# Performance work log

Hardware: AMD Instinct MI355X
Metric: run time of the kernel (lower is better)

Reference implementation:

```python
import jax, jax.numpy as jnp
import numpy as np

N = 100000
E = 1600000
D_IN = 128
D_H = 128


def _glorot(key, shape):
    fan_in, fan_out = shape[1], shape[0]
    lim = np.sqrt(6.0 / (fan_in + fan_out))
    return jax.random.uniform(key, shape, jnp.float32, -lim, lim)


def setup_inputs() -> dict:
    key = jax.random.key(0)
    ks = jax.random.split(key, 12)
    x = jax.random.normal(ks[0], (N, D_IN), jnp.float32)
    edge_index = jax.random.randint(ks[1], (2, E), 0, N, jnp.int64)
    return {
        "x": x,
        "edge_index": edge_index,
        # lin1, lin2 (nn.Linear: y = x @ W.T + b)
        "W1": _glorot(ks[2], (D_H, D_IN)),
        "b1": jnp.zeros((D_H,), jnp.float32),
        "W2": _glorot(ks[3], (D_H, D_H)),
        "b2": jnp.zeros((D_H,), jnp.float32),
        # SAGEConv1: lin_l (neighbors, with bias), lin_r (root, no bias)
        "c1_Wl": _glorot(ks[4], (D_H, D_H)),
        "c1_bl": jnp.zeros((D_H,), jnp.float32),
        "c1_Wr": _glorot(ks[5], (D_H, D_H)),
        # SAGEConv2
        "c2_Wl": _glorot(ks[6], (D_H, D_H)),
        "c2_bl": jnp.zeros((D_H,), jnp.float32),
        "c2_Wr": _glorot(ks[7], (D_H, D_H)),
    }


def _sage_conv(h, src, dst, Wl, bl, Wr, num_nodes):
    # PyG SAGEConv (mean aggr): out = lin_l(mean_{j in N(i)} h_j) + lin_r(h_i)
    msgs = h[src]  # [E, D] gather
    agg = jax.ops.segment_sum(msgs, dst, num_segments=num_nodes)  # [N, D]
    deg = jax.ops.segment_sum(jnp.ones((src.shape[0],), h.dtype), dst,
                              num_segments=num_nodes)
    mean = agg / jnp.maximum(deg, 1.0)[:, None]
    return mean @ Wl.T + bl + h @ Wr.T


def reference(x, edge_index, W1, b1, W2, b2,
              c1_Wl, c1_bl, c1_Wr, c2_Wl, c2_bl, c2_Wr):
    src, dst = edge_index[0], edge_index[1]
    n = x.shape[0]
    h = jax.nn.relu(x @ W1.T + b1)
    h = jax.nn.relu(_sage_conv(h, src, dst, c1_Wl, c1_bl, c1_Wr, n))
    h = jax.nn.relu(h @ W2.T + b2)
    h = jax.nn.relu(_sage_conv(h, src, dst, c2_Wl, c2_bl, c2_Wr, n))
    return h
```

## Files before the change

kernel.cpp:

```cpp
#include <hip/hip_runtime.h>
#include <hip/hip_bf16.h>

#define NN 100000
#define EE 1600000
#define DD 128

#define BSH 9
#define NBUK ((NN + 511) / 512)
#define EPB 8192
#define PGRID ((EE + EPB - 1) / EPB)

typedef __attribute__((ext_vector_type(8))) _Float16 half8;
typedef __attribute__((ext_vector_type(4))) _Float16 half4;
typedef __attribute__((ext_vector_type(2))) _Float16 half2v;
typedef __attribute__((ext_vector_type(4))) float f32x4;

__device__ inline int detect64(const long long* __restrict__ ei64) {
    long long v = ei64[threadIdx.x & 63];
    return __all(v >= 0 && v < (long long)NN);
}

__device__ inline int load_edge(const int* ei32, const long long* ei64, int is64, size_t pos) {
    return is64 ? (int)ei64[pos] : ei32[pos];
}

__global__ __launch_bounds__(1024) void k_bhist(const int* __restrict__ ei32,
                                                const long long* __restrict__ ei64,
                                                int* __restrict__ bh) {
    __shared__ int h[NBUK];
    int t = threadIdx.x;
    int is64 = detect64(ei64);
    if (t < NBUK) h[t] = 0;
    __syncthreads();
    int base = blockIdx.x * EPB;
    int end = min(base + EPB, EE);
    for (int e = base + t; e < end; e += 1024) {
        int d = load_edge(ei32, ei64, is64, (size_t)EE + e);
        atomicAdd(&h[d >> BSH], 1);
    }
    __syncthreads();
    if (t < NBUK) bh[blockIdx.x * 256 + t] = h[t];
}

__global__ __launch_bounds__(256) void k_bscan(const int* __restrict__ bh,
                                               int* __restrict__ bbase,
                                               int* __restrict__ bcur) {
    __shared__ int sm[256];
    int t = threadIdx.x;
    int v = 0;
    if (t < NBUK)
        for (int b = 0; b < PGRID; ++b) v += bh[b * 256 + t];
    sm[t] = v;
    __syncthreads();
    for (int off = 1; off < 256; off <<= 1) {
        int u = (t >= off) ? sm[t - off] : 0;
        __syncthreads();
        sm[t] += u;
        __syncthreads();
    }
    if (t < NBUK) {
        int b = sm[t] - v;
        bbase[t] = b;
        bcur[t] = b;
    }
    if (t == 0) bbase[NBUK] = EE;
}

__global__ __launch_bounds__(1024) void k_part(const int* __restrict__ ei32,
                                               const long long* __restrict__ ei64,
                                               int* __restrict__ bcur,
                                               unsigned* __restrict__ eb) {
    __shared__ int h[NBUK];
    __shared__ int cbase[NBUK];
    int t = threadIdx.x;
    int is64 = detect64(ei64);
    if (t < NBUK) h[t] = 0;
    __syncthreads();
    int base = blockIdx.x * EPB;
    int end = min(base + EPB, EE);
    for (int e = base + t; e < end; e += 1024) {
        int d = load_edge(ei32, ei64, is64, (size_t)EE + e);
        atomicAdd(&h[d >> BSH], 1);
    }
    __syncthreads();
    if (t < NBUK && h[t] > 0) cbase[t] = atomicAdd(&bcur[t], h[t]);
    __syncthreads();
    if (t < NBUK) h[t] = 0;
    __syncthreads();
    for (int e = base + t; e < end; e += 1024) {
        int s = load_edge(ei32, ei64, is64, (size_t)e);
        int d = load_edge(ei32, ei64, is64, (size_t)EE + e);
        int b = d >> BSH;
        int slot = atomicAdd(&h[b], 1);
        eb[cbase[b] + slot] = (unsigned)s | ((unsigned)(d & 511) << 17);
    }
}

__global__ __launch_bounds__(1024) void k_bucket(const unsigned* __restrict__ eb,
                                                 const int* __restrict__ bbase,
                                                 int* __restrict__ rp,
                                                 int* __restrict__ ssrc) {
    __shared__ int ncnt[512];
    __shared__ int cur[512];
    int b = blockIdx.x, t = threadIdx.x;
    int ebeg = bbase[b], eend = bbase[b + 1];
    int nodeBase = b << BSH;
    int nNodes = min(512, NN - nodeBase);
    if (t < 512) ncnt[t] = 0;
    __syncthreads();
    for (int i = ebeg + t; i < eend; i += 1024) {
        unsigned v = eb[i];
        atomicAdd(&ncnt[v >> 17], 1);
    }
    __syncthreads();
    int own = (t < 512) ? ncnt[t] : 0;
    for (int off = 1; off < 512; off <<= 1) {
        int u = (t >= off && t < 512) ? ncnt[t - off] : 0;
        __syncthreads();
        if (t < 512) ncnt[t] += u;
        __syncthreads();
    }
    if (t < 512) {
        int excl = ncnt[t] - own;
        cur[t] = ebeg + excl;
        if (t < nNodes) rp[nodeBase + t] = ebeg + excl;
    }
    __syncthreads();
    for (int i = ebeg + t; i < eend; i += 1024) {
        unsigned v = eb[i];
        int slot = atomicAdd(&cur[v >> 17], 1);
        ssrc[slot] = (int)(v & 0x1FFFFu);
    }
    if (b == 0 && t == 0) rp[NN] = EE;
}

#define WSTR 136

__device__ inline void stageW(const float* __restrict__ Wg, _Float16* sW, int t) {
#pragma unroll
    for (int i = 0; i < 16; ++i) {
        int c = t + i * 256;
        int n = c >> 5, j = c & 31;
        float4 w = ((const float4*)Wg)[c];
        half4 o;
        o[0] = (_Float16)w.x; o[1] = (_Float16)w.y;
        o[2] = (_Float16)w.z; o[3] = (_Float16)w.w;
        *(half4*)(sW + n * WSTR + j * 4) = o;
    }
}

template <bool DUAL, bool AF16, bool OF16>
__global__ __launch_bounds__(256) void k_gemm(const void* __restrict__ A,
                                              const float* __restrict__ W1g,
                                              const void* __restrict__ A2,
                                              const float* __restrict__ W2g,
                                              const float* __restrict__ bias,
                                              void* __restrict__ out) {
    __shared__ _Float16 sW[128 * WSTR];
    int t = threadIdx.x;
    int wave = t >> 6;
    int lane = t & 63;
    int lr = lane & 15;
    int lk = lane >> 4;
    int rowBase = blockIdx.x * 128 + wave * 32;

    f32x4 acc[2][8];
#pragma unroll
    for (int mt = 0; mt < 2; ++mt)
#pragma unroll
        for (int nt = 0; nt < 8; ++nt) acc[mt][nt] = (f32x4){0.f, 0.f, 0.f, 0.f};

    const int NPASS = DUAL ? 2 : 1;
    for (int pass = 0; pass < NPASS; ++pass) {
        const float* Wg = pass ? W2g : W1g;
        const void* Ap = pass ? A2 : A;
        if (pass) __syncthreads();
        stageW(Wg, sW, t);
        __syncthreads();

#pragma unroll
        for (int ks = 0; ks < 4; ++ks) {
            int kf = ks * 32 + lk * 8;
            half8 b[8];
#pragma unroll
            for (int nt = 0; nt < 8; ++nt)
                b[nt] = *(const half8*)(sW + (nt * 16 + lr) * WSTR + kf);
#pragma unroll
            for (int mt = 0; mt < 2; ++mt) {
                int row = rowBase + mt * 16 + lr;
                int rc = row < NN ? row : NN - 1;
                if (AF16) {
                    half8 a = *(const half8*)((const _Float16*)Ap + (size_t)rc * 128 + kf);
#pragma unroll
                    for (int nt = 0; nt < 8; ++nt)
                        acc[mt][nt] = __builtin_amdgcn_mfma_f32_16x16x32_f16(a, b[nt], acc[mt][nt], 0, 0, 0);
                } else {
                    const float* ap = (const float*)Ap + (size_t)rc * 128 + kf;
                    float4 a0 = *(const float4*)ap;
                    float4 a1 = *(const float4*)(ap + 4);
                    float av[8] = {a0.x, a0.y, a0.z, a0.w, a1.x, a1.y, a1.z, a1.w};
                    half8 ah, al;
#pragma unroll
                    for (int j = 0; j < 8; ++j) {
                        _Float16 h = (_Float16)av[j];
                        ah[j] = h;
                        al[j] = (_Float16)(av[j] - (float)h);
                    }
#pragma unroll
                    for (int nt = 0; nt < 8; ++nt) {
                        acc[mt][nt] = __builtin_amdgcn_mfma_f32_16x16x32_f16(ah, b[nt], acc[mt][nt], 0, 0, 0);
                        acc[mt][nt] = __builtin_amdgcn_mfma_f32_16x16x32_f16(al, b[nt], acc[mt][nt], 0, 0, 0);
                    }
                }
            }
        }
    }

#pragma unroll
    for (int mt = 0; mt < 2; ++mt) {
#pragma unroll
        for (int nt = 0; nt < 8; ++nt) {
            int col = nt * 16 + lr;
            float b = bias[col];
#pragma unroll
            for (int r = 0; r < 4; ++r) {
                int row = rowBase + mt * 16 + lk * 4 + r;
                if (row < NN) {
                    float v = acc[mt][nt][r] + b;
                    v = v > 0.f ? v : 0.f;
                    if (OF16)
                        ((_Float16*)out)[(size_t)row * 128 + col] = (_Float16)v;
                    else
                        ((float*)out)[(size_t)row * 128 + col] = v;
                }
            }
        }
    }
}

__global__ __launch_bounds__(256) void k_agg(const _Float16* __restrict__ h,
                                             const int* __restrict__ rp,
                                             const int* __restrict__ ssrc,
                                             _Float16* __restrict__ out) {
    int wid = (int)((blockIdx.x * 256 + threadIdx.x) >> 6);
    int lane = threadIdx.x & 63;
    if (wid >= NN) return;
    int g = lane >> 4;
    int f = lane & 15;
    int s = __builtin_amdgcn_readfirstlane(rp[wid]);
    int e = __builtin_amdgcn_readfirstlane(rp[wid + 1]);
    int deg = e - s;

    const half2v ONE = {(_Float16)1.f, (_Float16)1.f};
    const half2v ZER = {(_Float16)0.f, (_Float16)0.f};
    float fa[8] = {0.f, 0.f, 0.f, 0.f, 0.f, 0.f, 0.f, 0.f};

    for (int j = s; j < e; j += 16) {
        int j0 = j + g, j1 = j + 4 + g, j2 = j + 8 + g, j3 = j + 12 + g;
        int r0 = ssrc[j0 < e ? j0 : s];
        int r1 = ssrc[j1 < e ? j1 : s];
        int r2 = ssrc[j2 < e ? j2 : s];
        int r3 = ssrc[j3 < e ? j3 : s];
        half8 v0 = *(const half8*)(h + (size_t)r0 * 128 + f * 8);
        half8 v1 = *(const half8*)(h + (size_t)r1 * 128 + f * 8);
        half8 v2 = *(const half8*)(h + (size_t)r2 * 128 + f * 8);
        half8 v3 = *(const half8*)(h + (size_t)r3 * 128 + f * 8);
        if (j + 16 <= e) {
#pragma unroll
            for (int q = 0; q < 4; ++q) {
                half2v p0 = {v0[2 * q], v0[2 * q + 1]};
                half2v p1 = {v1[2 * q], v1[2 * q + 1]};
                half2v p2 = {v2[2 * q], v2[2 * q + 1]};
                half2v p3 = {v3[2 * q], v3[2 * q + 1]};
                half2v sA = p0 + p1;
                half2v sB = p2 + p3;
                fa[2 * q]     += (float)sA.x + (float)sB.x;
                fa[2 * q + 1] += (float)sA.y + (float)sB.y;
            }
        } else {
            half2v m0 = j0 < e ? ONE : ZER;
            half2v m1 = j1 < e ? ONE : ZER;
            half2v m2 = j2 < e ? ONE : ZER;
            half2v m3 = j3 < e ? ONE : ZER;
#pragma unroll
            for (int q = 0; q < 4; ++q) {
                half2v p0 = {v0[2 * q], v0[2 * q + 1]};
                half2v p1 = {v1[2 * q], v1[2 * q + 1]};
                half2v p2 = {v2[2 * q], v2[2 * q + 1]};
                half2v p3 = {v3[2 * q], v3[2 * q + 1]};
                half2v sA = p0 * m0 + p1 * m1;
                half2v sB = p2 * m2 + p3 * m3;
                fa[2 * q]     += (float)sA.x + (float)sB.x;
                fa[2 * q + 1] += (float)sA.y + (float)sB.y;
            }
        }
    }
#pragma unroll
    for (int q = 0; q < 8; ++q) {
        fa[q] += __shfl_xor(fa[q], 16, 64);
        fa[q] += __shfl_xor(fa[q], 32, 64);
    }
    float inv = deg > 0 ? 1.0f / (float)deg : 0.f;
    if (g == 0) {
        half8 o;
#pragma unroll
        for (int q = 0; q < 8; ++q) o[q] = (_Float16)(fa[q] * inv);
        *(half8*)(out + (size_t)wid * 128 + f * 8) = o;
    }
}

extern "C" void kernel_launch(void* const* d_in, const int* in_sizes, int n_in,
                              void* d_out, int out_size, void* d_ws, size_t ws_size,
                              hipStream_t stream) {
    const float* x = (const float*)d_in[0];
    const int* ei32 = (const int*)d_in[1];
    const long long* ei64 = (const long long*)d_in[1];
    const float* W1 = (const float*)d_in[2];
    const float* b1 = (const float*)d_in[3];
    const float* W2 = (const float*)d_in[4];
    const float* b2 = (const float*)d_in[5];
    const float* c1Wl = (const float*)d_in[6];
    const float* c1_bl = (const float*)d_in[7];
    const float* c1Wr = (const float*)d_in[8];
    const float* c2Wl = (const float*)d_in[9];
    const float* c2_bl = (const float*)d_in[10];
    const float* c2Wr = (const float*)d_in[11];

    char* ws = (char*)d_ws;
    const size_t H16 = (size_t)NN * 128 * 2;
    _Float16* hH = (_Float16*)ws;
    _Float16* aggH = (_Float16*)(ws + H16);
    int* ssrc = (int*)(ws + 2 * H16);
    int* rp = (int*)(ws + 2 * H16 + 6400000);
    int* bh = (int*)(ws + 2 * H16 + 6400000 + 400128);
    int* bbase = bh + PGRID * 256;
    int* bcur = bbase + 256;
    unsigned* eb = (unsigned*)hH;

    k_bhist<<<PGRID, 1024, 0, stream>>>(ei32, ei64, bh);
    k_bscan<<<1, 256, 0, stream>>>(bh, bbase, bcur);
    k_part<<<PGRID, 1024, 0, stream>>>(ei32, ei64, bcur, eb);
    k_bucket<<<NBUK, 1024, 0, stream>>>(eb, bbase, rp, ssrc);

    dim3 g((NN + 127) / 128);
    int agrid = (NN + 3) / 4;
    k_gemm<false, false, true><<<g, 256, 0, stream>>>(x, W1, nullptr, nullptr, b1, hH);
    k_agg<<<agrid, 256, 0, stream>>>(hH, rp, ssrc, aggH);
    k_gemm<true, true, true><<<g, 256, 0, stream>>>(aggH, c1Wl, hH, c1Wr, c1_bl, aggH);
    k_gemm<false, true, true><<<g, 256, 0, stream>>>(aggH, W2, nullptr, nullptr, b2, hH);
    k_agg<<<agrid, 256, 0, stream>>>(hH, rp, ssrc, aggH);
    k_gemm<true, true, false><<<g, 256, 0, stream>>>(aggH, c2Wl, hH, c2Wr, c2_bl, d_out);
}
```

Measured before the change: 420.5 us.

## Fuse SAGE conv1 with lin2 GEMM, pre-convert weights to fp16, atomic bucket histogram

Merges the first SAGE conv dual GEMM and the following lin2 GEMM into one kernel. The intermediate activation stays in shared memory, which removes one full N×128 fp16 write and read plus a kernel launch. All six weight matrices are converted to fp16 once in a prep kernel, so each GEMM block stages half-size weights without per-block conversion. The per-block bucket histogram is reduced with global atomics instead of a PGRID-long serial loop in the scan kernel, at the cost of a memset and extra launches. The fused kernel writes its output in place over aggH, which is safe only because each block reads just its own rows.

```diff
diff --git a/kernel.cpp b/kernel.cpp
--- a/kernel.cpp
+++ b/kernel.cpp
@@ -11,7 +11,6 @@
 #define PGRID ((EE + EPB - 1) / EPB)
 
 typedef __attribute__((ext_vector_type(8))) _Float16 half8;
-typedef __attribute__((ext_vector_type(4))) _Float16 half4;
 typedef __attribute__((ext_vector_type(2))) _Float16 half2v;
 typedef __attribute__((ext_vector_type(4))) float f32x4;
 
@@ -26,7 +25,7 @@
 
 __global__ __launch_bounds__(1024) void k_bhist(const int* __restrict__ ei32,
                                                 const long long* __restrict__ ei64,
-                                                int* __restrict__ bh) {
+                                                int* __restrict__ bcnt) {
     __shared__ int h[NBUK];
     int t = threadIdx.x;
     int is64 = detect64(ei64);
@@ -39,17 +38,15 @@
         atomicAdd(&h[d >> BSH], 1);
     }
     __syncthreads();
-    if (t < NBUK) bh[blockIdx.x * 256 + t] = h[t];
-}
-
-__global__ __launch_bounds__(256) void k_bscan(const int* __restrict__ bh,
+    if (t < NBUK && h[t] > 0) atomicAdd(&bcnt[t], h[t]);
+}
+
+__global__ __launch_bounds__(256) void k_bscan(const int* __restrict__ bcnt,
                                                int* __restrict__ bbase,
                                                int* __restrict__ bcur) {
     __shared__ int sm[256];
     int t = threadIdx.x;
-    int v = 0;
-    if (t < NBUK)
-        for (int b = 0; b < PGRID; ++b) v += bh[b * 256 + t];
+    int v = (t < NBUK) ? bcnt[t] : 0;
     sm[t] = v;
     __syncthreads();
     for (int off = 1; off < 256; off <<= 1) {
@@ -134,26 +131,34 @@
     if (b == 0 && t == 0) rp[NN] = EE;
 }
 
+__global__ void k_prepw(const float* __restrict__ w0, const float* __restrict__ w1,
+                        const float* __restrict__ w2, const float* __restrict__ w3,
+                        const float* __restrict__ w4, const float* __restrict__ w5,
+                        _Float16* __restrict__ whi) {
+    int i = blockIdx.x * 256 + threadIdx.x;
+    if (i >= 6 * 16384) return;
+    int slot = i >> 14, idx = i & 16383;
+    const float* w = slot == 0 ? w0 : slot == 1 ? w1 : slot == 2 ? w2
+                   : slot == 3 ? w3 : slot == 4 ? w4 : w5;
+    whi[i] = (_Float16)w[idx];
+}
+
 #define WSTR 136
 
-__device__ inline void stageW(const float* __restrict__ Wg, _Float16* sW, int t) {
-#pragma unroll
-    for (int i = 0; i < 16; ++i) {
+__device__ inline void stageW16(const _Float16* __restrict__ Wg, _Float16* sW, int t) {
+#pragma unroll
+    for (int i = 0; i < 8; ++i) {
         int c = t + i * 256;
-        int n = c >> 5, j = c & 31;
-        float4 w = ((const float4*)Wg)[c];
-        half4 o;
-        o[0] = (_Float16)w.x; o[1] = (_Float16)w.y;
-        o[2] = (_Float16)w.z; o[3] = (_Float16)w.w;
-        *(half4*)(sW + n * WSTR + j * 4) = o;
+        int n = c >> 4, j = c & 15;
+        *(half8*)(sW + n * WSTR + j * 8) = *(const half8*)(Wg + n * 128 + j * 8);
     }
 }
 
 template <bool DUAL, bool AF16, bool OF16>
 __global__ __launch_bounds__(256) void k_gemm(const void* __restrict__ A,
-                                              const float* __restrict__ W1g,
+                                              const _Float16* __restrict__ W1g,
                                               const void* __restrict__ A2,
-                                              const float* __restrict__ W2g,
+                                              const _Float16* __restrict__ W2g,
                                               const float* __restrict__ bias,
                                               void* __restrict__ out) {
     __shared__ _Float16 sW[128 * WSTR];
@@ -172,10 +177,10 @@
 
     const int NPASS = DUAL ? 2 : 1;
     for (int pass = 0; pass < NPASS; ++pass) {
-        const float* Wg = pass ? W2g : W1g;
+        const _Float16* Wg = pass ? W2g : W1g;
         const void* Ap = pass ? A2 : A;
         if (pass) __syncthreads();
-        stageW(Wg, sW, t);
+        stageW16(Wg, sW, t);
         __syncthreads();
 
 #pragma unroll
@@ -236,6 +241,121 @@
             }
         }
     }
+}
+
+__global__ __launch_bounds__(256) void k_cfuse(const _Float16* __restrict__ aggH,
+                                               const _Float16* __restrict__ rootH,
+                                               const _Float16* __restrict__ Wlg,
+                                               const _Float16* __restrict__ Wrg,
+                                               const float* __restrict__ bconv,
+                                               const _Float16* __restrict__ Wling,
+                                               const float* __restrict__ blin,
+                                               _Float16* __restrict__ out) {
+    __shared__ _Float16 sW[128 * WSTR];
+    __shared__ _Float16 sA[128 * WSTR];
+    int t = threadIdx.x;
+    int wave = t >> 6, lane = t & 63;
+    int lr = lane & 15, lk = lane >> 4;
+    int rowBase = blockIdx.x * 128 + wave * 32;
+
+    f32x4 acc[2][8];
+#pragma unroll
+    for (int mt = 0; mt < 2; ++mt)
+#pragma unroll
+        for (int nt = 0; nt < 8; ++nt) acc[mt][nt] = (f32x4){0.f, 0.f, 0.f, 0.f};
+
+    stageW16(Wlg, sW, t);
+    __syncthreads();
+#pragma unroll
+    for (int ks = 0; ks < 4; ++ks) {
+        int kf = ks * 32 + lk * 8;
+        half8 b[8];
+#pragma unroll
+        for (int nt = 0; nt < 8; ++nt)
+            b[nt] = *(const half8*)(sW + (nt * 16 + lr) * WSTR + kf);
+#pragma unroll
+        for (int mt = 0; mt < 2; ++mt) {
+            int row = rowBase + mt * 16 + lr;
+            int rc = row < NN ? row : NN - 1;
+            half8 a = *(const half8*)(aggH + (size_t)rc * 128 + kf);
+#pragma unroll
+            for (int nt = 0; nt < 8; ++nt)
+                acc[mt][nt] = __builtin_amdgcn_mfma_f32_16x16x32_f16(a, b[nt], acc[mt][nt], 0, 0, 0);
+        }
+    }
+    __syncthreads();
+
+    stageW16(Wrg, sW, t);
+    __syncthreads();
+#pragma unroll
+    for (int ks = 0; ks < 4; ++ks) {
+        int kf = ks * 32 + lk * 8;
+        half8 b[8];
+#pragma unroll
+        for (int nt = 0; nt < 8; ++nt)
+            b[nt] = *(const half8*)(sW + (nt * 16 + lr) * WSTR + kf);
+#pragma unroll
+        for (int mt = 0; mt < 2; ++mt) {
+            int row = rowBase + mt * 16 + lr;
+            int rc = row < NN ? row : NN - 1;
+            half8 a = *(const half8*)(rootH + (size_t)rc * 128 + kf);
+#pragma unroll
+            for (int nt = 0; nt < 8; ++nt)
+                acc[mt][nt] = __builtin_amdgcn_mfma_f32_16x16x32_f16(a, b[nt], acc[mt][nt], 0, 0, 0);
+        }
+    }
+
+#pragma unroll
+    for (int mt = 0; mt < 2; ++mt)
+#pragma unroll
+        for (int nt = 0; nt < 8; ++nt) {
+            int col = nt * 16 + lr;
+            float bia = bconv[col];
+#pragma unroll
+            for (int r = 0; r < 4; ++r) {
+                float v = acc[mt][nt][r] + bia;
+                sA[(wave * 32 + mt * 16 + lk * 4 + r) * WSTR + col] = (_Float16)(v > 0.f ? v : 0.f);
+            }
+        }
+    __syncthreads();
+
+    stageW16(Wling, sW, t);
+    __syncthreads();
+#pragma unroll
+    for (int mt = 0; mt < 2; ++mt)
+#pragma unroll
+        for (int nt = 0; nt < 8; ++nt) acc[mt][nt] = (f32x4){0.f, 0.f, 0.f, 0.f};
+#pragma unroll
+    for (int ks = 0; ks < 4; ++ks) {
+        int kf = ks * 32 + lk * 8;
+        half8 b[8];
+#pragma unroll
+        for (int nt = 0; nt < 8; ++nt)
+            b[nt] = *(const half8*)(sW + (nt * 16 + lr) * WSTR + kf);
+#pragma unroll
+        for (int mt = 0; mt < 2; ++mt) {
+            half8 a = *(const half8*)(sA + (wave * 32 + mt * 16 + lr) * WSTR + kf);
+#pragma unroll
+            for (int nt = 0; nt < 8; ++nt)
+                acc[mt][nt] = __builtin_amdgcn_mfma_f32_16x16x32_f16(a, b[nt], acc[mt][nt], 0, 0, 0);
+        }
+    }
+
+#pragma unroll
+    for (int mt = 0; mt < 2; ++mt)
+#pragma unroll
+        for (int nt = 0; nt < 8; ++nt) {
+            int col = nt * 16 + lr;
+            float bia = blin[col];
+#pragma unroll
+            for (int r = 0; r < 4; ++r) {
+                int row = rowBase + mt * 16 + lk * 4 + r;
+                if (row < NN) {
+                    float v = acc[mt][nt][r] + bia;
+                    out[(size_t)row * 128 + col] = (_Float16)(v > 0.f ? v : 0.f);
+                }
+            }
+        }
 }
 
 __global__ __launch_bounds__(256) void k_agg(const _Float16* __restrict__ h,
@@ -272,10 +392,10 @@
                 half2v p1 = {v1[2 * q], v1[2 * q + 1]};
                 half2v p2 = {v2[2 * q], v2[2 * q + 1]};
                 half2v p3 = {v3[2 * q], v3[2 * q + 1]};
-                half2v sA = p0 + p1;
-                half2v sB = p2 + p3;
-                fa[2 * q]     += (float)sA.x + (float)sB.x;
-                fa[2 * q + 1] += (float)sA.y + (float)sB.y;
+                half2v sA2 = p0 + p1;
+                half2v sB2 = p2 + p3;
+                fa[2 * q]     += (float)sA2.x + (float)sB2.x;
+                fa[2 * q + 1] += (float)sA2.y + (float)sB2.y;
             }
         } else {
             half2v m0 = j0 < e ? ONE : ZER;
@@ -288,10 +408,10 @@
                 half2v p1 = {v1[2 * q], v1[2 * q + 1]};
                 half2v p2 = {v2[2 * q], v2[2 * q + 1]};
                 half2v p3 = {v3[2 * q], v3[2 * q + 1]};
-                half2v sA = p0 * m0 + p1 * m1;
-                half2v sB = p2 * m2 + p3 * m3;
-                fa[2 * q]     += (float)sA.x + (float)sB.x;
-                fa[2 * q + 1] += (float)sA.y + (float)sB.y;
+                half2v sA2 = p0 * m0 + p1 * m1;
+                half2v sB2 = p2 * m2 + p3 * m3;
+                fa[2 * q]     += (float)sA2.x + (float)sB2.x;
+                fa[2 * q + 1] += (float)sA2.y + (float)sB2.y;
             }
         }
     }
@@ -315,16 +435,10 @@
     const float* x = (const float*)d_in[0];
     const int* ei32 = (const int*)d_in[1];
     const long long* ei64 = (const long long*)d_in[1];
-    const float* W1 = (const float*)d_in[2];
     const float* b1 = (const float*)d_in[3];
-    const float* W2 = (const float*)d_in[4];
     const float* b2 = (const float*)d_in[5];
-    const float* c1Wl = (const float*)d_in[6];
     const float* c1_bl = (const float*)d_in[7];
-    const float* c1Wr = (const float*)d_in[8];
-    const float* c2Wl = (const float*)d_in[9];
     const float* c2_bl = (const float*)d_in[10];
-    const float* c2Wr = (const float*)d_in[11];
 
     char* ws = (char*)d_ws;
     const size_t H16 = (size_t)NN * 128 * 2;
@@ -332,22 +446,32 @@
     _Float16* aggH = (_Float16*)(ws + H16);
     int* ssrc = (int*)(ws + 2 * H16);
     int* rp = (int*)(ws + 2 * H16 + 6400000);
-    int* bh = (int*)(ws + 2 * H16 + 6400000 + 400128);
-    int* bbase = bh + PGRID * 256;
-    int* bcur = bbase + 256;
+    int* bufs = (int*)(ws + 2 * H16 + 6400000 + 400128);
+    _Float16* whi = (_Float16*)(ws + 2 * H16 + 6400000 + 2 * 400128);
+
+    int* bcnt = bufs;
+    int* bbase = bufs + 256;
+    int* bcur = bufs + 512;
     unsigned* eb = (unsigned*)hH;
 
-    k_bhist<<<PGRID, 1024, 0, stream>>>(ei32, ei64, bh);
-    k_bscan<<<1, 256, 0, stream>>>(bh, bbase, bcur);
+    hipMemsetAsync(bcnt, 0, NBUK * 4, stream);
+    k_bhist<<<PGRID, 1024, 0, stream>>>(ei32, ei64, bcnt);
+    k_bscan<<<1, 256, 0, stream>>>(bcnt, bbase, bcur);
     k_part<<<PGRID, 1024, 0, stream>>>(ei32, ei64, bcur, eb);
     k_bucket<<<NBUK, 1024, 0, stream>>>(eb, bbase, rp, ssrc);
+    k_prepw<<<(6 * 16384 + 255) / 256, 256, 0, stream>>>(
+        (const float*)d_in[2], (const float*)d_in[6], (const float*)d_in[8],
+        (const float*)d_in[4], (const float*)d_in[9], (const float*)d_in[11], whi);
 
     dim3 g((NN + 127) / 128);
     int agrid = (NN + 3) / 4;
-    k_gemm<false, false, true><<<g, 256, 0, stream>>>(x, W1, nullptr, nullptr, b1, hH);
+    k_gemm<false, false, true><<<g, 256, 0, stream>>>(
+        x, whi + 0 * 16384, nullptr, nullptr, b1, hH);
     k_agg<<<agrid, 256, 0, stream>>>(hH, rp, ssrc, aggH);
-    k_gemm<true, true, true><<<g, 256, 0, stream>>>(aggH, c1Wl, hH, c1Wr, c1_bl, aggH);
-    k_gemm<false, true, true><<<g, 256, 0, stream>>>(aggH, W2, nullptr, nullptr, b2, hH);
-    k_agg<<<agrid, 256, 0, stream>>>(hH, rp, ssrc, aggH);
-    k_gemm<true, true, false><<<g, 256, 0, stream>>>(aggH, c2Wl, hH, c2Wr, c2_bl, d_out);
-}
+    k_cfuse<<<g, 256, 0, stream>>>(
+        aggH, hH, whi + 1 * 16384, whi + 2 * 16384, c1_bl,
+        whi + 3 * 16384, b2, aggH);
+    k_agg<<<agrid, 256, 0, stream>>>(aggH, rp, ssrc, hH);
+    k_gemm<true, true, false><<<g, 256, 0, stream>>>(
+        hH, whi + 4 * 16384, aggH, whi + 5 * 16384, c2_bl, d_out);
+}
```

New measurement: 367.5 us. -12.6%, faster.
